# Kernel optimization log

Hardware: AMD Instinct MI355X
Metric: run time of the kernel (lower is better)

The kernel has to match this reference:

```python
import jax, jax.numpy as jnp
import numpy as np

N, D = 16384, 256
T = 0.5
C = 100


def setup_inputs() -> dict:
    key = jax.random.key(0)
    x = jax.random.normal(key, (N, D), dtype=jnp.float32)
    # L2-normalize rows (standard for contrastive embeddings; also keeps
    # exp(sim/T) in fp32 range, matching the module's intended use)
    x = x / jnp.linalg.norm(x, axis=1, keepdims=True)
    return {"x": x}


def reference(x) -> jnp.ndarray:
    # sim[i,j] = <x_i, x_j> / T ; loss = (1/C) * sum_i log(sum_j exp(sim[i,j]))
    sim = jnp.exp(jnp.matmul(x, x.T) / T)          # [N, N]
    row = jnp.log(jnp.sum(sim, axis=1))            # [N]
    return jnp.sum(row) / C                        # scalar
```

## Files before the change

kernel.cpp:

```cpp
#include <hip/hip_runtime.h>
#include <hip/hip_bf16.h>
#include <math.h>


#define N_ROWS 16384
#define KD     256
#define NT     64
#define NTILE  (NT * (NT + 1) / 2)
#define NBLK   512
#define NSLOT  96

#define SCALE_SQRT 1.6986436f

typedef short short8 __attribute__((ext_vector_type(8)));
typedef float f32x4  __attribute__((ext_vector_type(4)));

typedef __attribute__((address_space(3))) void       lds_void;
typedef const __attribute__((address_space(1))) void gm_void;

__device__ __forceinline__ float fast_exp2(float x) {
#if __has_builtin(__builtin_amdgcn_exp2f)
    return __builtin_amdgcn_exp2f(x);
#else
    return exp2f(x);
#endif
}

__device__ __forceinline__ void gll16(const void* g, void* l) {
    __builtin_amdgcn_global_load_lds((gm_void*)g, (lds_void*)l, 16, 0, 0);
}

__global__ void convert_kernel(const float* __restrict__ x, unsigned short* __restrict__ xb,
                               float* __restrict__ rowacc, float* __restrict__ out) {
    const int bx = blockIdx.x, tid = threadIdx.x;
    if (bx < (NSLOT * N_ROWS) / 1024)
        *(float4*)(rowacc + (size_t)(bx * 256 + tid) * 4) = (float4){0.f, 0.f, 0.f, 0.f};
    if (bx == 2000 && tid == 0) out[0] = 0.f;
    int i = (bx * 256 + tid) * 4;
    float4 v = *(const float4*)(x + i);
    ushort4 o;
    {
        unsigned int u;
        u = __float_as_uint(v.x * SCALE_SQRT); u += 0x7fff + ((u >> 16) & 1); o.x = (unsigned short)(u >> 16);
        u = __float_as_uint(v.y * SCALE_SQRT); u += 0x7fff + ((u >> 16) & 1); o.y = (unsigned short)(u >> 16);
        u = __float_as_uint(v.z * SCALE_SQRT); u += 0x7fff + ((u >> 16) & 1); o.z = (unsigned short)(u >> 16);
        u = __float_as_uint(v.w * SCALE_SQRT); u += 0x7fff + ((u >> 16) & 1); o.w = (unsigned short)(u >> 16);
    }
    *(ushort4*)(xb + i) = o;
}

__global__ __launch_bounds__(256, 2)
void simloss_main(const unsigned short* __restrict__ xb, float* __restrict__ rowacc) {
    __shared__ __align__(128) char smem[65536 + 1024 + 4096];
    float* const rowred = (float*)(smem + 65536);
    float* const colred = (float*)(smem + 65536 + 1024);

    const int tid  = threadIdx.x;
    const int lane = tid & 63;
    const int w    = tid >> 6;
    const int l15  = lane & 15;
    const int lg   = lane >> 4;
    const int b    = blockIdx.x;

    int t          = (b * 65) >> 4;
    const int tEnd = ((b + 1) * 65) >> 4;
    const int rowSlot = NT + (b & 31);

    int rb = (int)((sqrtf(8.f * (float)t + 1.f) - 1.f) * 0.5f);
    while ((rb + 1) * (rb + 2) / 2 <= t) ++rb;
    while (rb * (rb + 1) / 2 > t) --rb;

    #pragma unroll 1
    while (t < tEnd) {
        while ((rb + 1) * (rb + 2) / 2 <= t) ++rb;
        const int rowStart = rb * (rb + 1) / 2;
        const int cb0 = t - rowStart;
        const int tE  = tEnd - rowStart;
        const int cbE = tE < rb + 1 ? tE : rb + 1;
        const int NI  = (cbE - cb0) * 4;
        const int r0  = rb * 256;
        const int colblk0 = cb0 * 4;

        auto stageB = [&](int buf, int cblk) {
            const unsigned short* s = xb + (size_t)(cblk * 64 + w * 16 + l15) * KD + lg * 8;
            char* dst = smem + buf * 32768 + (w * 8) * 1024;
            #pragma unroll
            for (int kt = 0; kt < 8; ++kt)
                gll16(s + kt * 32, dst + kt * 1024);
        };
        stageB(0, colblk0);

        short8 afrag[4][8];
        #pragma unroll
        for (int m = 0; m < 4; ++m) {
            const unsigned short* ar = xb + (size_t)(r0 + w * 64 + m * 16 + l15) * KD + lg * 8;
            #pragma unroll
            for (int kt = 0; kt < 8; ++kt)
                afrag[m][kt] = *(const short8*)(ar + kt * 32);
        }
        #pragma unroll
        for (int m = 0; m < 4; ++m)
            #pragma unroll
            for (int kt = 0; kt < 8; ++kt)
                asm volatile("" : "+v"(afrag[m][kt]));

        float rowsum[4][4] = {{0.f}};

        #pragma unroll 1
        for (int fi = 0; fi < NI; ++fi) {
            const int cur = fi & 1;
            if (fi + 1 < NI) {
                stageB(cur ^ 1, colblk0 + fi + 1);
                asm volatile("s_waitcnt vmcnt(8)" ::: "memory");
            } else {
                asm volatile("s_waitcnt vmcnt(0)" ::: "memory");
            }
            __builtin_amdgcn_s_barrier();
            asm volatile("" ::: "memory");

            const char* bbase = smem + cur * 32768;
            #pragma unroll
            for (int ct = 0; ct < 4; ++ct) {
                short8 bfrag[8];
                #pragma unroll
                for (int kt = 0; kt < 8; ++kt)
                    bfrag[kt] = *(const short8*)(bbase + (ct * 8 + kt) * 1024 + lane * 16);
                f32x4 acc[4];
                #pragma unroll
                for (int m = 0; m < 4; ++m) acc[m] = (f32x4){0.f, 0.f, 0.f, 0.f};
                #pragma unroll
                for (int kt = 0; kt < 8; ++kt)
                    #pragma unroll
                    for (int m = 0; m < 4; ++m)
                        acc[m] = __builtin_amdgcn_mfma_f32_16x16x32_bf16(afrag[m][kt], bfrag[kt], acc[m], 0, 0, 0);
                float csum = 0.f;
                #pragma unroll
                for (int m = 0; m < 4; ++m)
                    #pragma unroll
                    for (int r = 0; r < 4; ++r) {
                        float e = fast_exp2(acc[m][r]);
                        rowsum[m][r] += e;
                        csum += e;
                    }
                csum += __shfl_xor(csum, 16);
                csum += __shfl_xor(csum, 32);
                if (lg == 0)
                    colred[w * 256 + (fi & 3) * 64 + ct * 16 + l15] = csum;
            }

            asm volatile("" ::: "memory");
            __builtin_amdgcn_s_barrier();
            asm volatile("" ::: "memory");

            if ((fi & 3) == 3) {
                const int cb = cb0 + (fi >> 2);
                if (cb != rb) {
                    float cs = colred[tid] + colred[256 + tid] + colred[512 + tid] + colred[768 + tid];
                    rowacc[(size_t)rb * N_ROWS + cb * 256 + tid] = cs;
                }
            }
        }

        #pragma unroll
        for (int m = 0; m < 4; ++m)
            #pragma unroll
            for (int r = 0; r < 4; ++r) {
                float v = rowsum[m][r];
                v += __shfl_xor(v, 1);
                v += __shfl_xor(v, 2);
                v += __shfl_xor(v, 4);
                v += __shfl_xor(v, 8);
                if (l15 == 0) rowred[w * 64 + m * 16 + lg * 4 + r] = v;
            }
        __syncthreads();
        rowacc[(size_t)rowSlot * N_ROWS + r0 + tid] = rowred[tid];

        t = rowStart + cbE;
    }
}

__global__ void finalize_kernel(const float* __restrict__ rowacc, float* __restrict__ out) {
    int i = blockIdx.x * 256 + threadIdx.x;
    float s = 0.f;
    #pragma unroll 8
    for (int k = 0; k < NSLOT; ++k) s += rowacc[(size_t)k * N_ROWS + i];
    float v = logf(s);
    #pragma unroll
    for (int off = 1; off < 64; off <<= 1) v += __shfl_xor(v, off);
    __shared__ float red[4];
    if ((threadIdx.x & 63) == 0) red[threadIdx.x >> 6] = v;
    __syncthreads();
    if (threadIdx.x == 0)
        atomicAdd(out, (red[0] + red[1] + red[2] + red[3]) * 0.01f);
}

extern "C" void kernel_launch(void* const* d_in, const int* in_sizes, int n_in,
                              void* d_out, int out_size, void* d_ws, size_t ws_size,
                              hipStream_t stream) {
    const float* x = (const float*)d_in[0];
    unsigned short* xb = (unsigned short*)d_ws;
    float* rowacc = (float*)((char*)d_ws + (size_t)N_ROWS * KD * 2);
    float* out = (float*)d_out;

    convert_kernel<<<(N_ROWS * KD) / (256 * 4), 256, 0, stream>>>(x, xb, rowacc, out);
    simloss_main<<<NBLK, 256, 0, stream>>>(xb, rowacc);
    finalize_kernel<<<N_ROWS / 256, 256, 0, stream>>>(rowacc, out);
}
```

Before: 149.9 us.

## Switch main GEMM to 32x32x16 bf16 MFMA with matching fragment layouts

Replaces the 16x16x32 MFMA tiling with 32x32x16 MFMA instructions, so each wave computes two 32x32 accumulators per column tile. The A fragments, the LDS staging layout for B and the row and column reduction index mapping are rearranged to fit the 32x32 output layout. It also adds s_setprio around the MFMA bursts. The aim is fewer instructions and fewer LDS fragment reads per FLOP. In exchange the accumulators get larger, which adds register pressure, and the rowsum index remapping must be exactly right.

```diff
diff --git a/kernel.cpp b/kernel.cpp
--- a/kernel.cpp
+++ b/kernel.cpp
@@ -6,14 +6,13 @@
 #define N_ROWS 16384
 #define KD     256
 #define NT     64
-#define NTILE  (NT * (NT + 1) / 2)
 #define NBLK   512
 #define NSLOT  96
 
 #define SCALE_SQRT 1.6986436f
 
 typedef short short8 __attribute__((ext_vector_type(8)));
-typedef float f32x4  __attribute__((ext_vector_type(4)));
+typedef float f32x16 __attribute__((ext_vector_type(16)));
 
 typedef __attribute__((address_space(3))) void       lds_void;
 typedef const __attribute__((address_space(1))) void gm_void;
@@ -58,8 +57,8 @@
     const int tid  = threadIdx.x;
     const int lane = tid & 63;
     const int w    = tid >> 6;
-    const int l15  = lane & 15;
-    const int lg   = lane >> 4;
+    const int l31  = lane & 31;
+    const int lh   = lane >> 5;
     const int b    = blockIdx.x;
 
     int t          = (b * 65) >> 4;
@@ -82,29 +81,34 @@
         const int colblk0 = cb0 * 4;
 
         auto stageB = [&](int buf, int cblk) {
-            const unsigned short* s = xb + (size_t)(cblk * 64 + w * 16 + l15) * KD + lg * 8;
-            char* dst = smem + buf * 32768 + (w * 8) * 1024;
-            #pragma unroll
-            for (int kt = 0; kt < 8; ++kt)
-                gll16(s + kt * 32, dst + kt * 1024);
+            #pragma unroll
+            for (int g = 0; g < 8; ++g) {
+                const int fr = w * 8 + g;
+                const int ct = fr >> 4, kt = fr & 15;
+                const unsigned short* s =
+                    xb + (size_t)(cblk * 64 + ct * 32 + l31) * KD + kt * 16 + lh * 8;
+                gll16(s, smem + buf * 32768 + fr * 1024);
+            }
         };
         stageB(0, colblk0);
 
-        short8 afrag[4][8];
-        #pragma unroll
-        for (int m = 0; m < 4; ++m) {
-            const unsigned short* ar = xb + (size_t)(r0 + w * 64 + m * 16 + l15) * KD + lg * 8;
-            #pragma unroll
-            for (int kt = 0; kt < 8; ++kt)
-                afrag[m][kt] = *(const short8*)(ar + kt * 32);
+        short8 af[2][16];
+        #pragma unroll
+        for (int m = 0; m < 2; ++m) {
+            const unsigned short* ar = xb + (size_t)(r0 + w * 64 + m * 32 + l31) * KD + lh * 8;
+            #pragma unroll
+            for (int kt = 0; kt < 16; ++kt)
+                af[m][kt] = *(const short8*)(ar + kt * 16);
         }
         #pragma unroll
-        for (int m = 0; m < 4; ++m)
-            #pragma unroll
-            for (int kt = 0; kt < 8; ++kt)
-                asm volatile("" : "+v"(afrag[m][kt]));
-
-        float rowsum[4][4] = {{0.f}};
+        for (int m = 0; m < 2; ++m)
+            #pragma unroll
+            for (int kt = 0; kt < 16; ++kt)
+                asm volatile("" : "+v"(af[m][kt]));
+
+        float rowsum[32];
+        #pragma unroll
+        for (int r = 0; r < 32; ++r) rowsum[r] = 0.f;
 
         #pragma unroll 1
         for (int fi = 0; fi < NI; ++fi) {
@@ -120,32 +124,33 @@
 
             const char* bbase = smem + cur * 32768;
             #pragma unroll
-            for (int ct = 0; ct < 4; ++ct) {
-                short8 bfrag[8];
+            for (int ct = 0; ct < 2; ++ct) {
+                f32x16 acc0, acc1;
                 #pragma unroll
-                for (int kt = 0; kt < 8; ++kt)
-                    bfrag[kt] = *(const short8*)(bbase + (ct * 8 + kt) * 1024 + lane * 16);
-                f32x4 acc[4];
+                for (int r = 0; r < 16; ++r) { acc0[r] = 0.f; acc1[r] = 0.f; }
                 #pragma unroll
-                for (int m = 0; m < 4; ++m) acc[m] = (f32x4){0.f, 0.f, 0.f, 0.f};
-                #pragma unroll
-                for (int kt = 0; kt < 8; ++kt)
+                for (int q = 0; q < 4; ++q) {
+                    short8 bf[4];
                     #pragma unroll
-                    for (int m = 0; m < 4; ++m)
-                        acc[m] = __builtin_amdgcn_mfma_f32_16x16x32_bf16(afrag[m][kt], bfrag[kt], acc[m], 0, 0, 0);
+                    for (int j = 0; j < 4; ++j)
+                        bf[j] = *(const short8*)(bbase + (ct * 16 + q * 4 + j) * 1024 + lane * 16);
+                    __builtin_amdgcn_s_setprio(1);
+                    #pragma unroll
+                    for (int j = 0; j < 4; ++j) {
+                        acc0 = __builtin_amdgcn_mfma_f32_32x32x16_bf16(af[0][q * 4 + j], bf[j], acc0, 0, 0, 0);
+                        acc1 = __builtin_amdgcn_mfma_f32_32x32x16_bf16(af[1][q * 4 + j], bf[j], acc1, 0, 0, 0);
+                    }
+                    __builtin_amdgcn_s_setprio(0);
+                }
                 float csum = 0.f;
                 #pragma unroll
-                for (int m = 0; m < 4; ++m)
-                    #pragma unroll
-                    for (int r = 0; r < 4; ++r) {
-                        float e = fast_exp2(acc[m][r]);
-                        rowsum[m][r] += e;
-                        csum += e;
-                    }
-                csum += __shfl_xor(csum, 16);
+                for (int r = 0; r < 16; ++r) {
+                    float e0 = fast_exp2(acc0[r]); rowsum[r]      += e0; csum += e0;
+                    float e1 = fast_exp2(acc1[r]); rowsum[16 + r] += e1; csum += e1;
+                }
                 csum += __shfl_xor(csum, 32);
-                if (lg == 0)
-                    colred[w * 256 + (fi & 3) * 64 + ct * 16 + l15] = csum;
+                if (lh == 0)
+                    colred[w * 256 + (fi & 3) * 64 + ct * 32 + l31] = csum;
             }
 
             asm volatile("" ::: "memory");
@@ -162,15 +167,17 @@
         }
 
         #pragma unroll
-        for (int m = 0; m < 4; ++m)
-            #pragma unroll
-            for (int r = 0; r < 4; ++r) {
-                float v = rowsum[m][r];
+        for (int m = 0; m < 2; ++m)
+            #pragma unroll
+            for (int r = 0; r < 16; ++r) {
+                float v = rowsum[m * 16 + r];
                 v += __shfl_xor(v, 1);
                 v += __shfl_xor(v, 2);
                 v += __shfl_xor(v, 4);
                 v += __shfl_xor(v, 8);
-                if (l15 == 0) rowred[w * 64 + m * 16 + lg * 4 + r] = v;
+                v += __shfl_xor(v, 16);
+                if (l31 == 0)
+                    rowred[w * 64 + m * 32 + (r & 3) + 8 * (r >> 2) + 4 * lh] = v;
             }
         __syncthreads();
         rowacc[(size_t)rowSlot * N_ROWS + r0 + tid] = rowred[tid];
```

New measurement: 186.2 us. 1.24x slower.

## Use 512-row bands with 8-wave blocks and 4-deep B-tile pipeline

Applied to the files above, without the earlier changes.

Restructures the symmetric-tile schedule into 512-row bands handled by 512-thread blocks (8 waves), so each staged B column block is reused across twice as many rows. B staging becomes a 4-buffer ring with two tiles in flight. Column-sum reduction is deferred by one iteration into a double-buffered colred area, which removes the second barrier per iteration. It uses 128KB+ of LDS per block and halves the grid to 256 blocks, which may limit occupancy and load balance.

```diff
diff --git a/kernel.cpp b/kernel.cpp
--- a/kernel.cpp
+++ b/kernel.cpp
@@ -5,9 +5,9 @@
 
 #define N_ROWS 16384
 #define KD     256
-#define NT     64
-#define NTILE  (NT * (NT + 1) / 2)
-#define NBLK   512
+#define NBAND  32
+#define FI_TOTAL 4224
+#define NBLK   256
 #define NSLOT  96
 
 #define SCALE_SQRT 1.6986436f
@@ -49,11 +49,11 @@
     *(ushort4*)(xb + i) = o;
 }
 
-__global__ __launch_bounds__(256, 2)
+__global__ __launch_bounds__(512, 2)
 void simloss_main(const unsigned short* __restrict__ xb, float* __restrict__ rowacc) {
-    __shared__ __align__(128) char smem[65536 + 1024 + 4096];
-    float* const rowred = (float*)(smem + 65536);
-    float* const colred = (float*)(smem + 65536 + 1024);
+    __shared__ __align__(128) char smem[4 * 32768 + 2048 + 4096];
+    float* const rowred = (float*)(smem + 131072);
+    float* const colred = (float*)(smem + 131072 + 2048);
 
     const int tid  = threadIdx.x;
     const int lane = tid & 63;
@@ -62,33 +62,37 @@
     const int lg   = lane >> 4;
     const int b    = blockIdx.x;
 
-    int t          = (b * 65) >> 4;
-    const int tEnd = ((b + 1) * 65) >> 4;
-    const int rowSlot = NT + (b & 31);
-
-    int rb = (int)((sqrtf(8.f * (float)t + 1.f) - 1.f) * 0.5f);
-    while ((rb + 1) * (rb + 2) / 2 <= t) ++rb;
-    while (rb * (rb + 1) / 2 > t) --rb;
+    int f          = (b * 33) >> 1;
+    const int fEnd = ((b + 1) * 33) >> 1;
+    const int rowSlot = 64 + (b & 31);
+
+    int rb = (int)((sqrtf((float)f + 1.f) - 1.f) * 0.5f);
+    while (4 * (rb + 1) * (rb + 2) <= f) ++rb;
+    while (4 * rb * (rb + 1) > f) --rb;
 
     #pragma unroll 1
-    while (t < tEnd) {
-        while ((rb + 1) * (rb + 2) / 2 <= t) ++rb;
-        const int rowStart = rb * (rb + 1) / 2;
-        const int cb0 = t - rowStart;
-        const int tE  = tEnd - rowStart;
-        const int cbE = tE < rb + 1 ? tE : rb + 1;
-        const int NI  = (cbE - cb0) * 4;
-        const int r0  = rb * 256;
-        const int colblk0 = cb0 * 4;
+    while (f < fEnd) {
+        while (4 * (rb + 1) * (rb + 2) <= f) ++rb;
+        const int bandStart = 4 * rb * (rb + 1);
+        const int cblk0   = f - bandStart;
+        const int bandEnd = bandStart + 8 * (rb + 1);
+        const int lim = fEnd < bandEnd ? fEnd : bandEnd;
+        const int NI  = lim - f;
+        const int r0  = rb * 512;
 
         auto stageB = [&](int buf, int cblk) {
-            const unsigned short* s = xb + (size_t)(cblk * 64 + w * 16 + l15) * KD + lg * 8;
-            char* dst = smem + buf * 32768 + (w * 8) * 1024;
-            #pragma unroll
-            for (int kt = 0; kt < 8; ++kt)
-                gll16(s + kt * 32, dst + kt * 1024);
+            if (cblk > 255) cblk = 255;
+            #pragma unroll
+            for (int g = 0; g < 4; ++g) {
+                const int fr = w * 4 + g;
+                const int ct = fr >> 3, kt = fr & 7;
+                const unsigned short* s =
+                    xb + (size_t)(cblk * 64 + ct * 16 + l15) * KD + kt * 32 + lg * 8;
+                gll16(s, smem + buf * 32768 + fr * 1024);
+            }
         };
-        stageB(0, colblk0);
+        stageB(0, cblk0);
+        stageB(1, cblk0 + 1);
 
         short8 afrag[4][8];
         #pragma unroll
@@ -108,17 +112,31 @@
 
         #pragma unroll 1
         for (int fi = 0; fi < NI; ++fi) {
-            const int cur = fi & 1;
-            if (fi + 1 < NI) {
-                stageB(cur ^ 1, colblk0 + fi + 1);
+            if (fi + 2 < NI) {
+                stageB((fi + 2) & 3, cblk0 + fi + 2);
                 asm volatile("s_waitcnt vmcnt(8)" ::: "memory");
+            } else if (fi + 1 < NI) {
+                asm volatile("s_waitcnt vmcnt(4)" ::: "memory");
             } else {
                 asm volatile("s_waitcnt vmcnt(0)" ::: "memory");
             }
+            asm volatile("s_waitcnt lgkmcnt(0)" ::: "memory");
             __builtin_amdgcn_s_barrier();
             asm volatile("" ::: "memory");
 
-            const char* bbase = smem + cur * 32768;
+            if (fi > 0 && tid < 64) {
+                const int pc = cblk0 + fi - 1;
+                if (pc < rb * 8) {
+                    const float* cp = colred + ((fi - 1) & 1) * 512;
+                    float cs = 0.f;
+                    #pragma unroll
+                    for (int w2 = 0; w2 < 8; ++w2) cs += cp[w2 * 64 + tid];
+                    rowacc[(size_t)rb * N_ROWS + pc * 64 + tid] = cs;
+                }
+            }
+
+            const char* bbase = smem + (fi & 3) * 32768;
+            float* cw = colred + (fi & 1) * 512;
             #pragma unroll
             for (int ct = 0; ct < 4; ++ct) {
                 short8 bfrag[8];
@@ -144,20 +162,21 @@
                     }
                 csum += __shfl_xor(csum, 16);
                 csum += __shfl_xor(csum, 32);
-                if (lg == 0)
-                    colred[w * 256 + (fi & 3) * 64 + ct * 16 + l15] = csum;
-            }
-
+                if (lg == 0) cw[w * 64 + ct * 16 + l15] = csum;
+            }
             asm volatile("" ::: "memory");
-            __builtin_amdgcn_s_barrier();
-            asm volatile("" ::: "memory");
-
-            if ((fi & 3) == 3) {
-                const int cb = cb0 + (fi >> 2);
-                if (cb != rb) {
-                    float cs = colred[tid] + colred[256 + tid] + colred[512 + tid] + colred[768 + tid];
-                    rowacc[(size_t)rb * N_ROWS + cb * 256 + tid] = cs;
-                }
+        }
+
+        __syncthreads();
+
+        if (tid < 64) {
+            const int pc = cblk0 + NI - 1;
+            if (pc < rb * 8) {
+                const float* cp = colred + ((NI - 1) & 1) * 512;
+                float cs = 0.f;
+                #pragma unroll
+                for (int w2 = 0; w2 < 8; ++w2) cs += cp[w2 * 64 + tid];
+                rowacc[(size_t)rb * N_ROWS + pc * 64 + tid] = cs;
             }
         }
 
@@ -175,7 +194,7 @@
         __syncthreads();
         rowacc[(size_t)rowSlot * N_ROWS + r0 + tid] = rowred[tid];
 
-        t = rowStart + cbE;
+        f = lim;
     }
 }
 
@@ -203,6 +222,6 @@
     float* out = (float*)d_out;
 
     convert_kernel<<<(N_ROWS * KD) / (256 * 4), 256, 0, stream>>>(x, xb, rowacc, out);
-    simloss_main<<<NBLK, 256, 0, stream>>>(xb, rowacc);
+    simloss_main<<<NBLK, 512, 0, stream>>>(xb, rowacc);
     finalize_kernel<<<N_ROWS / 256, 256, 0, stream>>>(rowacc, out);
 }
```

Measured after the change: 149.9 us. No clear change (+0.0%).
